# Kernel optimization log

Measured on AMD Instinct MI355X. Metric: run time of the kernel, lower is better.

Reference implementation:

```python
import jax, jax.numpy as jnp
import numpy as np

B, S, D_IN, D_OUT = 16, 2048, 512, 64
N_SLOTS = 1000  # faithful to original kernel shape; only slices 0..2 used
SCALE = 1.0 / jnp.sqrt(jnp.float32(64.0))


def setup_inputs() -> dict:
    key = jax.random.key(0)
    k1, k2 = jax.random.split(key)
    inputs = jax.random.normal(k1, (B, S, D_IN), dtype=jnp.float32)
    # keras 'uniform' initializer: U(-0.05, 0.05)
    kernel = jax.random.uniform(k2, (N_SLOTS, D_IN, D_OUT), dtype=jnp.float32,
                                minval=-0.05, maxval=0.05)
    return {"inputs": inputs, "kernel": kernel}


def reference(inputs, kernel):
    # Q, K, V projections: [B,S,D_in] @ [D_in,D_out] -> [B,S,D_out]
    q = jnp.einsum('bsi,io->bso', inputs, kernel[0])
    k = jnp.einsum('bsi,io->bso', inputs, kernel[1])
    v = jnp.einsum('bsi,io->bso', inputs, kernel[2])
    # scores: [B,S,S], scaled by 1/sqrt(64)
    scores = jnp.einsum('bqd,bkd->bqk', q, k) * SCALE
    attn = jax.nn.softmax(scores, axis=-1)
    # output: [B,S,D_out]
    return jnp.einsum('bqk,bkd->bqd', attn, v)
```

## Files before the change

### kernel.cpp

```cpp
#include <hip/hip_runtime.h>
#include <hip/hip_bf16.h>

typedef __bf16 bhalf;
typedef __attribute__((ext_vector_type(8)))  __bf16 bhalf8;
typedef __attribute__((ext_vector_type(4)))  float  f32x4;
typedef __attribute__((ext_vector_type(16))) float  f32x16;
typedef __attribute__((ext_vector_type(4)))  unsigned int u32x4;

#define NB   16
#define SEQ  2048
#define DIN  512
#define DOUT 64
#define NTOK (NB*SEQ)
#define NSPLIT 4
#define KVPER (SEQ/NSPLIT)

#define WT_BYTES (192*512*2)
#define Q_OFF    ((size_t)WT_BYTES)
#define QKV_BYTES ((size_t)NTOK*DOUT*2)
#define K_OFF    (Q_OFF + QKV_BYTES)
#define VT_OFF   (K_OFF + QKV_BYTES)

__device__ __forceinline__ void gl_lds16(const void* g, void* l) {
  __builtin_amdgcn_global_load_lds(
      (const __attribute__((address_space(1))) void*)g,
      (__attribute__((address_space(3))) void*)l, 16, 0, 0);
}

__global__ __launch_bounds__(256) void prep_w(const float* __restrict__ wk,
                                              bhalf* __restrict__ wt) {
  int tid  = blockIdx.x*256 + threadIdx.x;
  int slot = tid >> 15;
  int rem  = tid & 32767;
  int k    = rem >> 6;
  int col  = rem & 63;
  float v  = wk[tid];
  if (slot == 0) v *= 0.18033688011112042f;
  wt[(size_t)(slot*64 + col)*DIN + k] = (bhalf)v;
}

__global__ __launch_bounds__(256) void proj_qkv(const float* __restrict__ x,
    const bhalf* __restrict__ wt, bhalf* __restrict__ qb,
    bhalf* __restrict__ kb, bhalf* __restrict__ vtb) {
  __shared__ __align__(16) char smem[81920];
  char* const xs  = smem;
  char* const wsl = smem + 32768;

  const int tid  = threadIdx.x;
  const int lane = tid & 63;
  const int wv   = tid >> 6;
  const int r16  = lane & 15;
  const int g    = lane >> 4;
  const int tok0 = blockIdx.x * 64;

  const char* const xg = (const char*)(x + (size_t)tok0 * DIN);
  const char* const wg = (const char*)wt;

  auto stage = [&](int buf, int c) {
#pragma unroll
    for (int i = 0; i < 10; ++i) {
      const int p = wv*10 + i;
      if (p < 24) {
        const int n = p*8 + (lane >> 3);
        const int s = lane & 7;
        gl_lds16(wg + (size_t)n*1024 + c*128 + ((s ^ (n & 7)) << 4),
                 wsl + buf*24576 + p*1024);
      } else {
        const int q = p - 24;
        const int r = q*4 + (lane >> 4);
        const int s = lane & 15;
        gl_lds16(xg + (size_t)r*2048 + c*256 + ((s ^ (r & 7)) << 4),
                 xs + buf*16384 + q*1024);
      }
    }
  };

  f32x4 acc[12];
#pragma unroll
  for (int i = 0; i < 12; ++i) acc[i] = (f32x4){0.f, 0.f, 0.f, 0.f};

  stage(0, 0);
  __syncthreads();

  const int row = wv*16 + r16;
  const int rx7 = r16 & 7;

  int buf = 0;
  for (int c = 0; c < 8; ++c) {
    if (c < 7) stage(buf ^ 1, c + 1);
    const char* xrow = xs  + buf*16384 + row*256;
    const char* wb   = wsl + buf*24576;
#pragma unroll
    for (int kk = 0; kk < 2; ++kk) {
      const int sa = kk*8 + g*2;
      f32x4 xa = *(const f32x4*)(xrow + (( sa      ^ rx7) << 4));
      f32x4 xc = *(const f32x4*)(xrow + (((sa + 1) ^ rx7) << 4));
      bhalf8 a;
      a[0]=(bhalf)xa[0]; a[1]=(bhalf)xa[1]; a[2]=(bhalf)xa[2]; a[3]=(bhalf)xa[3];
      a[4]=(bhalf)xc[0]; a[5]=(bhalf)xc[1]; a[6]=(bhalf)xc[2]; a[7]=(bhalf)xc[3];
      const int sb = (kk*4 + g) ^ rx7;
      __builtin_amdgcn_s_setprio(1);
#pragma unroll
      for (int nt = 0; nt < 12; ++nt) {
        const bhalf8 bf = *(const bhalf8*)(wb + (nt*16 + r16)*128 + (sb << 4));
        acc[nt] = __builtin_amdgcn_mfma_f32_16x16x32_bf16(a, bf, acc[nt], 0, 0, 0);
      }
      __builtin_amdgcn_s_setprio(0);
    }
    __syncthreads();
    buf ^= 1;
  }

#pragma unroll
  for (int nt = 0; nt < 8; ++nt) {
    bhalf* dst = (nt < 4) ? qb : kb;
    const size_t base = (size_t)(nt & 3)*512 + (size_t)(r16 >> 3)*256 + (r16 & 7);
#pragma unroll
    for (int rr = 0; rr < 4; ++rr) {
      const int tok = tok0 + wv*16 + g*4 + rr;
      dst[(size_t)(tok >> 5)*2048 + base + (tok & 31)*8] = (bhalf)acc[nt][rr];
    }
  }
  auto vlds = (bhalf(*)[64][24])(void*)smem;
#pragma unroll
  for (int nt = 8; nt < 12; ++nt)
#pragma unroll
    for (int rr = 0; rr < 4; ++rr)
      vlds[wv][(nt - 8)*16 + r16][g*4 + rr] = (bhalf)acc[nt][rr];
  __syncthreads();
  {
    const int f    = lane;
    const int tokG = tok0 + wv*16;
    const int tile = tokG >> 5;
    const int s    = (tokG >> 4) & 1;
    bhalf8 v0 = *(const bhalf8*)&vlds[wv][f][0];
    bhalf8 v1 = *(const bhalf8*)&vlds[wv][f][8];
    bhalf* dstv = vtb + (size_t)tile*2048 + (size_t)(f >> 5)*1024
                      + (size_t)s*512 + (size_t)(f & 31)*8;
    *(bhalf8*)dstv         = v0;
    *(bhalf8*)(dstv + 256) = v1;
  }
}

__device__ __forceinline__ unsigned cvtpk(float lo, float hi_) {
  unsigned r;
  asm("v_cvt_pk_bf16_f32 %0, %1, %2" : "=v"(r) : "v"(lo), "v"(hi_));
  return r;
}
__device__ __forceinline__ bhalf8 mk8(unsigned a, unsigned b, unsigned c, unsigned d) {
  u32x4 u; u[0]=a; u[1]=b; u[2]=c; u[3]=d;
  return __builtin_bit_cast(bhalf8, u);
}

__global__ __launch_bounds__(256, 4) void attn(const bhalf* __restrict__ qb,
    const bhalf* __restrict__ kb, const bhalf* __restrict__ vtb,
    float* __restrict__ out) {
  __shared__ float po[NSPLIT][64][33];
  __shared__ float pl[NSPLIT][32];

  const int lane = threadIdx.x & 63;
  const int wv   = threadIdx.x >> 6;
  const int l31  = lane & 31;
  const int hi   = lane >> 5;

  const int qtile = (blockIdx.x & 7)*128 + (blockIdx.x >> 3);
  const int qbase = qtile*32;
  const int b     = qbase >> 11;
  const int kv0   = wv * KVPER;
  const int tile0 = b*64 + wv*16;

  const int fo = hi*256 + l31*8;

  const bhalf* qpk = qb + (size_t)qtile*2048 + fo;
  const bhalf8 qf0 = *(const bhalf8*)(qpk);
  const bhalf8 qf1 = *(const bhalf8*)(qpk + 512);
  const bhalf8 qf2 = *(const bhalf8*)(qpk + 1024);
  const bhalf8 qf3 = *(const bhalf8*)(qpk + 1536);

  const bhalf* kpk = kb  + (size_t)tile0*2048 + fo;
  const bhalf* vpk = vtb + (size_t)tile0*2048 + fo;

  f32x16 ot0, ot1;
#pragma unroll
  for (int r = 0; r < 16; ++r) { ot0[r] = 0.f; ot1[r] = 0.f; }
  float lsum = 0.f;

  bhalf8 kf0, kf1, kf2, kf3;
  bhalf8 vf0, vf1, vf2, vf3;
  bhalf8 pf0, pf1;
  f32x16 s;

#define LOADK(IT) do { const bhalf* p_ = kpk + (IT)*2048;                       \
    kf0 = *(const bhalf8*)(p_);          kf1 = *(const bhalf8*)(p_ + 512);      \
    kf2 = *(const bhalf8*)(p_ + 1024);   kf3 = *(const bhalf8*)(p_ + 1536); } while (0)
#define LOADV(IT) do { const bhalf* p_ = vpk + (IT)*2048;                       \
    vf0 = *(const bhalf8*)(p_);          vf1 = *(const bhalf8*)(p_ + 512);      \
    vf2 = *(const bhalf8*)(p_ + 1024);   vf3 = *(const bhalf8*)(p_ + 1536); } while (0)
#define QK() do {                                                               \
    _Pragma("unroll") for (int r_ = 0; r_ < 16; ++r_) s[r_] = 0.f;              \
    __builtin_amdgcn_s_setprio(1);                                              \
    s = __builtin_amdgcn_mfma_f32_32x32x16_bf16(kf0, qf0, s, 0, 0, 0);          \
    s = __builtin_amdgcn_mfma_f32_32x32x16_bf16(kf1, qf1, s, 0, 0, 0);          \
    s = __builtin_amdgcn_mfma_f32_32x32x16_bf16(kf2, qf2, s, 0, 0, 0);          \
    s = __builtin_amdgcn_mfma_f32_32x32x16_bf16(kf3, qf3, s, 0, 0, 0);          \
    __builtin_amdgcn_s_setprio(0); } while (0)
#define SM() do {                                                               \
    _Pragma("unroll") for (int r_ = 0; r_ < 16; ++r_)                           \
      s[r_] = __builtin_amdgcn_exp2f(s[r_]);                                    \
    lsum += ((s[0]+s[1])+(s[2]+s[3])) + ((s[4]+s[5])+(s[6]+s[7]))               \
          + ((s[8]+s[9])+(s[10]+s[11])) + ((s[12]+s[13])+(s[14]+s[15]));        \
    unsigned w0 = cvtpk(s[0],  s[1]),  w1 = cvtpk(s[2],  s[3]);                 \
    unsigned w2 = cvtpk(s[4],  s[5]),  w3 = cvtpk(s[6],  s[7]);                 \
    unsigned w4 = cvtpk(s[8],  s[9]),  w5 = cvtpk(s[10], s[11]);                \
    unsigned w6 = cvtpk(s[12], s[13]), w7 = cvtpk(s[14], s[15]);                \
    asm volatile("v_permlane32_swap_b32 %0, %1" : "+v"(w0), "+v"(w2));          \
    asm volatile("v_permlane32_swap_b32 %0, %1" : "+v"(w1), "+v"(w3));          \
    asm volatile("v_permlane32_swap_b32 %0, %1" : "+v"(w4), "+v"(w6));          \
    asm volatile("v_permlane32_swap_b32 %0, %1" : "+v"(w5), "+v"(w7));          \
    pf0 = mk8(w0, w1, w2, w3);                                                  \
    pf1 = mk8(w4, w5, w6, w7); } while (0)
#define PV() do {                                                               \
    __builtin_amdgcn_s_setprio(1);                                              \
    ot0 = __builtin_amdgcn_mfma_f32_32x32x16_bf16(vf0, pf0, ot0, 0, 0, 0);      \
    ot0 = __builtin_amdgcn_mfma_f32_32x32x16_bf16(vf1, pf1, ot0, 0, 0, 0);      \
    ot1 = __builtin_amdgcn_mfma_f32_32x32x16_bf16(vf2, pf0, ot1, 0, 0, 0);      \
    ot1 = __builtin_amdgcn_mfma_f32_32x32x16_bf16(vf3, pf1, ot1, 0, 0, 0);      \
    __builtin_amdgcn_s_setprio(0); } while (0)

  LOADK(0);
  LOADV(0);
  QK();
  LOADK(1);
  SM();

  for (int it = 0; it < KVPER/32 - 1; ++it) {
    PV();
    LOADV(it + 1);
    QK();
    if (it < KVPER/32 - 2) LOADK(it + 2);
    SM();
  }
  PV();

#undef LOADK
#undef LOADV
#undef QK
#undef SM
#undef PV

  lsum += __shfl_xor(lsum, 32);

#pragma unroll
  for (int r = 0; r < 16; ++r) {
    int d0 = (r & 3) + 8*(r >> 2) + 4*hi;
    po[wv][d0][l31]      = ot0[r];
    po[wv][32 + d0][l31] = ot1[r];
  }
  if (hi == 0) pl[wv][l31] = lsum;
  __syncthreads();

  {
    int q  = threadIdx.x >> 3;
    int dg = (threadIdx.x & 7) * 8;
    float L  = pl[0][q] + pl[1][q] + pl[2][q] + pl[3][q];
    float inv = 1.0f / L;
    float* orow = out + (size_t)(qbase + q)*DOUT + dg;
#pragma unroll
    for (int j = 0; j < 8; ++j) {
      float acc = po[0][dg+j][q] + po[1][dg+j][q]
                + po[2][dg+j][q] + po[3][dg+j][q];
      orow[j] = acc * inv;
    }
  }
}

extern "C" void kernel_launch(void* const* d_in, const int* in_sizes, int n_in,
                              void* d_out, int out_size, void* d_ws, size_t ws_size,
                              hipStream_t stream) {
  const float* x  = (const float*)d_in[0];
  const float* wk = (const float*)d_in[1];
  float* out = (float*)d_out;

  char* ws = (char*)d_ws;
  bhalf* wt = (bhalf*)(ws);
  bhalf* qq = (bhalf*)(ws + Q_OFF);
  bhalf* kk = (bhalf*)(ws + K_OFF);
  bhalf* vt = (bhalf*)(ws + VT_OFF);

  prep_w  <<<dim3(384),  dim3(256), 0, stream>>>(wk, wt);
  proj_qkv<<<dim3(512),  dim3(256), 0, stream>>>(x, wt, qq, kk, vt);
  attn    <<<dim3(1024), dim3(256), 0, stream>>>(qq, kk, vt, out);
}
```

Before: 51.07 us.

## Process two query tiles per attention block and split projection N across 8 waves

Each attention block now handles two 32-row query tiles, so every K/V fragment loaded from global memory is reused for two QK/PV chains. The grid halves to 512 blocks and the loop interleaves the two chains' MFMAs and softmax to hide latency. The projection kernel moves to 512 threads, with two wave groups splitting the 12 output column tiles, which lowers per-wave accumulator pressure and raises parallelism. The cost is more registers in attention (occupancy hint removed) and fewer attention blocks, which could under-fill the GPU.

```diff
diff --git a/kernel.cpp b/kernel.cpp
--- a/kernel.cpp
+++ b/kernel.cpp
@@ -39,7 +39,7 @@
   wt[(size_t)(slot*64 + col)*DIN + k] = (bhalf)v;
 }
 
-__global__ __launch_bounds__(256) void proj_qkv(const float* __restrict__ x,
+__global__ __launch_bounds__(512) void proj_qkv(const float* __restrict__ x,
     const bhalf* __restrict__ wt, bhalf* __restrict__ qb,
     bhalf* __restrict__ kb, bhalf* __restrict__ vtb) {
   __shared__ __align__(16) char smem[81920];
@@ -49,6 +49,8 @@
   const int tid  = threadIdx.x;
   const int lane = tid & 63;
   const int wv   = tid >> 6;
+  const int tg   = wv & 3;
+  const int ng   = wv >> 2;
   const int r16  = lane & 15;
   const int g    = lane >> 4;
   const int tok0 = blockIdx.x * 64;
@@ -58,8 +60,8 @@
 
   auto stage = [&](int buf, int c) {
 #pragma unroll
-    for (int i = 0; i < 10; ++i) {
-      const int p = wv*10 + i;
+    for (int i = 0; i < 5; ++i) {
+      const int p = wv*5 + i;
       if (p < 24) {
         const int n = p*8 + (lane >> 3);
         const int s = lane & 7;
@@ -75,14 +77,13 @@
     }
   };
 
-  f32x4 acc[12];
-#pragma unroll
-  for (int i = 0; i < 12; ++i) acc[i] = (f32x4){0.f, 0.f, 0.f, 0.f};
+  f32x4 acc0 = {0.f,0.f,0.f,0.f}, acc1 = acc0, acc2 = acc0,
+        acc3 = acc0, acc4 = acc0, acc5 = acc0;
 
   stage(0, 0);
   __syncthreads();
 
-  const int row = wv*16 + r16;
+  const int row = tg*16 + r16;
   const int rx7 = r16 & 7;
 
   int buf = 0;
@@ -100,41 +101,48 @@
       a[4]=(bhalf)xc[0]; a[5]=(bhalf)xc[1]; a[6]=(bhalf)xc[2]; a[7]=(bhalf)xc[3];
       const int sb = (kk*4 + g) ^ rx7;
       __builtin_amdgcn_s_setprio(1);
-#pragma unroll
-      for (int nt = 0; nt < 12; ++nt) {
-        const bhalf8 bf = *(const bhalf8*)(wb + (nt*16 + r16)*128 + (sb << 4));
-        acc[nt] = __builtin_amdgcn_mfma_f32_16x16x32_bf16(a, bf, acc[nt], 0, 0, 0);
-      }
+#define MF(J, ACC) do {                                                         \
+        const int nt_ = ng*6 + (J);                                             \
+        const bhalf8 bf_ = *(const bhalf8*)(wb + (nt_*16 + r16)*128 + (sb << 4)); \
+        ACC = __builtin_amdgcn_mfma_f32_16x16x32_bf16(a, bf_, ACC, 0, 0, 0);    \
+      } while (0)
+      MF(0, acc0); MF(1, acc1); MF(2, acc2);
+      MF(3, acc3); MF(4, acc4); MF(5, acc5);
+#undef MF
       __builtin_amdgcn_s_setprio(0);
     }
     __syncthreads();
     buf ^= 1;
   }
 
-#pragma unroll
-  for (int nt = 0; nt < 8; ++nt) {
-    bhalf* dst = (nt < 4) ? qb : kb;
-    const size_t base = (size_t)(nt & 3)*512 + (size_t)(r16 >> 3)*256 + (r16 & 7);
-#pragma unroll
-    for (int rr = 0; rr < 4; ++rr) {
-      const int tok = tok0 + wv*16 + g*4 + rr;
-      dst[(size_t)(tok >> 5)*2048 + base + (tok & 31)*8] = (bhalf)acc[nt][rr];
-    }
-  }
+#define STOREJ(J, ACC) do {                                                     \
+    const int nt = ng*6 + (J);                                                  \
+    if (nt < 8) {                                                               \
+      bhalf* dst = (nt < 4) ? qb : kb;                                          \
+      const size_t base = (size_t)(nt & 3)*512 + (size_t)(r16 >> 3)*256 + (r16 & 7); \
+      _Pragma("unroll")                                                         \
+      for (int rr = 0; rr < 4; ++rr) {                                          \
+        const int tok = tok0 + tg*16 + g*4 + rr;                                \
+        dst[(size_t)(tok >> 5)*2048 + base + (tok & 31)*8] = (bhalf)ACC[rr];    \
+      }                                                                         \
+    } else {                                                                    \
+      _Pragma("unroll")                                                         \
+      for (int rr = 0; rr < 4; ++rr)                                            \
+        vlds[tg][(nt - 8)*16 + r16][g*4 + rr] = (bhalf)ACC[rr];                 \
+    } } while (0)
+
   auto vlds = (bhalf(*)[64][24])(void*)smem;
-#pragma unroll
-  for (int nt = 8; nt < 12; ++nt)
-#pragma unroll
-    for (int rr = 0; rr < 4; ++rr)
-      vlds[wv][(nt - 8)*16 + r16][g*4 + rr] = (bhalf)acc[nt][rr];
-  __syncthreads();
-  {
+  STOREJ(0, acc0); STOREJ(1, acc1); STOREJ(2, acc2);
+  STOREJ(3, acc3); STOREJ(4, acc4); STOREJ(5, acc5);
+#undef STOREJ
+  __syncthreads();
+  if (ng == 1) {
     const int f    = lane;
-    const int tokG = tok0 + wv*16;
+    const int tokG = tok0 + tg*16;
     const int tile = tokG >> 5;
     const int s    = (tokG >> 4) & 1;
-    bhalf8 v0 = *(const bhalf8*)&vlds[wv][f][0];
-    bhalf8 v1 = *(const bhalf8*)&vlds[wv][f][8];
+    bhalf8 v0 = *(const bhalf8*)&vlds[tg][f][0];
+    bhalf8 v1 = *(const bhalf8*)&vlds[tg][f][8];
     bhalf* dstv = vtb + (size_t)tile*2048 + (size_t)(f >> 5)*1024
                       + (size_t)s*512 + (size_t)(f & 31)*8;
     *(bhalf8*)dstv         = v0;
@@ -152,7 +160,7 @@
   return __builtin_bit_cast(bhalf8, u);
 }
 
-__global__ __launch_bounds__(256, 4) void attn(const bhalf* __restrict__ qb,
+__global__ __launch_bounds__(256) void attn(const bhalf* __restrict__ qb,
     const bhalf* __restrict__ kb, const bhalf* __restrict__ vtb,
     float* __restrict__ out) {
   __shared__ float po[NSPLIT][64][33];
@@ -163,31 +171,35 @@
   const int l31  = lane & 31;
   const int hi   = lane >> 5;
 
-  const int qtile = (blockIdx.x & 7)*128 + (blockIdx.x >> 3);
-  const int qbase = qtile*32;
-  const int b     = qbase >> 11;
-  const int kv0   = wv * KVPER;
+  const int pr    = (blockIdx.x & 7)*64 + (blockIdx.x >> 3);
+  const int qtA   = pr*2;
+  const int qtB   = qtA + 1;
+  const int b     = qtA >> 6;
   const int tile0 = b*64 + wv*16;
-
-  const int fo = hi*256 + l31*8;
-
-  const bhalf* qpk = qb + (size_t)qtile*2048 + fo;
-  const bhalf8 qf0 = *(const bhalf8*)(qpk);
-  const bhalf8 qf1 = *(const bhalf8*)(qpk + 512);
-  const bhalf8 qf2 = *(const bhalf8*)(qpk + 1024);
-  const bhalf8 qf3 = *(const bhalf8*)(qpk + 1536);
+  const int fo    = hi*256 + l31*8;
+
+  const bhalf* qpA = qb + (size_t)qtA*2048 + fo;
+  const bhalf8 qfA0 = *(const bhalf8*)(qpA);
+  const bhalf8 qfA1 = *(const bhalf8*)(qpA + 512);
+  const bhalf8 qfA2 = *(const bhalf8*)(qpA + 1024);
+  const bhalf8 qfA3 = *(const bhalf8*)(qpA + 1536);
+  const bhalf* qpB = qb + (size_t)qtB*2048 + fo;
+  const bhalf8 qfB0 = *(const bhalf8*)(qpB);
+  const bhalf8 qfB1 = *(const bhalf8*)(qpB + 512);
+  const bhalf8 qfB2 = *(const bhalf8*)(qpB + 1024);
+  const bhalf8 qfB3 = *(const bhalf8*)(qpB + 1536);
 
   const bhalf* kpk = kb  + (size_t)tile0*2048 + fo;
   const bhalf* vpk = vtb + (size_t)tile0*2048 + fo;
 
-  f32x16 ot0, ot1;
-#pragma unroll
-  for (int r = 0; r < 16; ++r) { ot0[r] = 0.f; ot1[r] = 0.f; }
-  float lsum = 0.f;
+  f32x16 otA0, otA1, otB0, otB1;
+#pragma unroll
+  for (int r = 0; r < 16; ++r) { otA0[r]=0.f; otA1[r]=0.f; otB0[r]=0.f; otB1[r]=0.f; }
+  float lsA = 0.f, lsB = 0.f;
 
   bhalf8 kf0, kf1, kf2, kf3;
   bhalf8 vf0, vf1, vf2, vf3;
-  bhalf8 pf0, pf1;
+  bhalf8 pfA0, pfA1, pfB0, pfB1;
   f32x16 s;
 
 #define LOADK(IT) do { const bhalf* p_ = kpk + (IT)*2048;                       \
@@ -196,19 +208,19 @@
 #define LOADV(IT) do { const bhalf* p_ = vpk + (IT)*2048;                       \
     vf0 = *(const bhalf8*)(p_);          vf1 = *(const bhalf8*)(p_ + 512);      \
     vf2 = *(const bhalf8*)(p_ + 1024);   vf3 = *(const bhalf8*)(p_ + 1536); } while (0)
-#define QK() do {                                                               \
+#define QK(QF0, QF1, QF2, QF3) do {                                             \
     _Pragma("unroll") for (int r_ = 0; r_ < 16; ++r_) s[r_] = 0.f;              \
     __builtin_amdgcn_s_setprio(1);                                              \
-    s = __builtin_amdgcn_mfma_f32_32x32x16_bf16(kf0, qf0, s, 0, 0, 0);          \
-    s = __builtin_amdgcn_mfma_f32_32x32x16_bf16(kf1, qf1, s, 0, 0, 0);          \
-    s = __builtin_amdgcn_mfma_f32_32x32x16_bf16(kf2, qf2, s, 0, 0, 0);          \
-    s = __builtin_amdgcn_mfma_f32_32x32x16_bf16(kf3, qf3, s, 0, 0, 0);          \
+    s = __builtin_amdgcn_mfma_f32_32x32x16_bf16(kf0, QF0, s, 0, 0, 0);          \
+    s = __builtin_amdgcn_mfma_f32_32x32x16_bf16(kf1, QF1, s, 0, 0, 0);          \
+    s = __builtin_amdgcn_mfma_f32_32x32x16_bf16(kf2, QF2, s, 0, 0, 0);          \
+    s = __builtin_amdgcn_mfma_f32_32x32x16_bf16(kf3, QF3, s, 0, 0, 0);          \
     __builtin_amdgcn_s_setprio(0); } while (0)
-#define SM() do {                                                               \
+#define SM(PF0, PF1, LS) do {                                                   \
     _Pragma("unroll") for (int r_ = 0; r_ < 16; ++r_)                           \
       s[r_] = __builtin_amdgcn_exp2f(s[r_]);                                    \
-    lsum += ((s[0]+s[1])+(s[2]+s[3])) + ((s[4]+s[5])+(s[6]+s[7]))               \
-          + ((s[8]+s[9])+(s[10]+s[11])) + ((s[12]+s[13])+(s[14]+s[15]));        \
+    LS += ((s[0]+s[1])+(s[2]+s[3])) + ((s[4]+s[5])+(s[6]+s[7]))                 \
+        + ((s[8]+s[9])+(s[10]+s[11])) + ((s[12]+s[13])+(s[14]+s[15]));          \
     unsigned w0 = cvtpk(s[0],  s[1]),  w1 = cvtpk(s[2],  s[3]);                 \
     unsigned w2 = cvtpk(s[4],  s[5]),  w3 = cvtpk(s[6],  s[7]);                 \
     unsigned w4 = cvtpk(s[8],  s[9]),  w5 = cvtpk(s[10], s[11]);                \
@@ -217,30 +229,29 @@
     asm volatile("v_permlane32_swap_b32 %0, %1" : "+v"(w1), "+v"(w3));          \
     asm volatile("v_permlane32_swap_b32 %0, %1" : "+v"(w4), "+v"(w6));          \
     asm volatile("v_permlane32_swap_b32 %0, %1" : "+v"(w5), "+v"(w7));          \
-    pf0 = mk8(w0, w1, w2, w3);                                                  \
-    pf1 = mk8(w4, w5, w6, w7); } while (0)
-#define PV() do {                                                               \
+    PF0 = mk8(w0, w1, w2, w3);                                                  \
+    PF1 = mk8(w4, w5, w6, w7); } while (0)
+#define PV(PF0, PF1, OT0, OT1) do {                                             \
     __builtin_amdgcn_s_setprio(1);                                              \
-    ot0 = __builtin_amdgcn_mfma_f32_32x32x16_bf16(vf0, pf0, ot0, 0, 0, 0);      \
-    ot0 = __builtin_amdgcn_mfma_f32_32x32x16_bf16(vf1, pf1, ot0, 0, 0, 0);      \
-    ot1 = __builtin_amdgcn_mfma_f32_32x32x16_bf16(vf2, pf0, ot1, 0, 0, 0);      \
-    ot1 = __builtin_amdgcn_mfma_f32_32x32x16_bf16(vf3, pf1, ot1, 0, 0, 0);      \
+    OT0 = __builtin_amdgcn_mfma_f32_32x32x16_bf16(vf0, PF0, OT0, 0, 0, 0);      \
+    OT0 = __builtin_amdgcn_mfma_f32_32x32x16_bf16(vf1, PF1, OT0, 0, 0, 0);      \
+    OT1 = __builtin_amdgcn_mfma_f32_32x32x16_bf16(vf2, PF0, OT1, 0, 0, 0);      \
+    OT1 = __builtin_amdgcn_mfma_f32_32x32x16_bf16(vf3, PF1, OT1, 0, 0, 0);      \
     __builtin_amdgcn_s_setprio(0); } while (0)
 
   LOADK(0);
   LOADV(0);
-  QK();
-  LOADK(1);
-  SM();
-
-  for (int it = 0; it < KVPER/32 - 1; ++it) {
-    PV();
-    LOADV(it + 1);
-    QK();
-    if (it < KVPER/32 - 2) LOADK(it + 2);
-    SM();
-  }
-  PV();
+
+  for (int it = 0; it < KVPER/32; ++it) {
+    QK(qfA0, qfA1, qfA2, qfA3);
+    SM(pfA0, pfA1, lsA);
+    QK(qfB0, qfB1, qfB2, qfB3);
+    if (it < KVPER/32 - 1) LOADK(it + 1);
+    PV(pfA0, pfA1, otA0, otA1);
+    SM(pfB0, pfB1, lsB);
+    PV(pfB0, pfB1, otB0, otB1);
+    if (it < KVPER/32 - 1) LOADV(it + 1);
+  }
 
 #undef LOADK
 #undef LOADV
@@ -248,29 +259,47 @@
 #undef SM
 #undef PV
 
-  lsum += __shfl_xor(lsum, 32);
+  lsA += __shfl_xor(lsA, 32);
+  lsB += __shfl_xor(lsB, 32);
 
 #pragma unroll
   for (int r = 0; r < 16; ++r) {
     int d0 = (r & 3) + 8*(r >> 2) + 4*hi;
-    po[wv][d0][l31]      = ot0[r];
-    po[wv][32 + d0][l31] = ot1[r];
-  }
-  if (hi == 0) pl[wv][l31] = lsum;
-  __syncthreads();
-
+    po[wv][d0][l31]      = otA0[r];
+    po[wv][32 + d0][l31] = otA1[r];
+  }
+  if (hi == 0) pl[wv][l31] = lsA;
+  __syncthreads();
   {
     int q  = threadIdx.x >> 3;
     int dg = (threadIdx.x & 7) * 8;
-    float L  = pl[0][q] + pl[1][q] + pl[2][q] + pl[3][q];
+    float L   = pl[0][q] + pl[1][q] + pl[2][q] + pl[3][q];
     float inv = 1.0f / L;
-    float* orow = out + (size_t)(qbase + q)*DOUT + dg;
-#pragma unroll
-    for (int j = 0; j < 8; ++j) {
-      float acc = po[0][dg+j][q] + po[1][dg+j][q]
-                + po[2][dg+j][q] + po[3][dg+j][q];
-      orow[j] = acc * inv;
-    }
+    float* orow = out + (size_t)(qtA*32 + q)*DOUT + dg;
+#pragma unroll
+    for (int j = 0; j < 8; ++j)
+      orow[j] = (po[0][dg+j][q] + po[1][dg+j][q]
+               + po[2][dg+j][q] + po[3][dg+j][q]) * inv;
+  }
+  __syncthreads();
+#pragma unroll
+  for (int r = 0; r < 16; ++r) {
+    int d0 = (r & 3) + 8*(r >> 2) + 4*hi;
+    po[wv][d0][l31]      = otB0[r];
+    po[wv][32 + d0][l31] = otB1[r];
+  }
+  if (hi == 0) pl[wv][l31] = lsB;
+  __syncthreads();
+  {
+    int q  = threadIdx.x >> 3;
+    int dg = (threadIdx.x & 7) * 8;
+    float L   = pl[0][q] + pl[1][q] + pl[2][q] + pl[3][q];
+    float inv = 1.0f / L;
+    float* orow = out + (size_t)(qtB*32 + q)*DOUT + dg;
+#pragma unroll
+    for (int j = 0; j < 8; ++j)
+      orow[j] = (po[0][dg+j][q] + po[1][dg+j][q]
+               + po[2][dg+j][q] + po[3][dg+j][q]) * inv;
   }
 }
 
@@ -287,7 +316,7 @@
   bhalf* kk = (bhalf*)(ws + K_OFF);
   bhalf* vt = (bhalf*)(ws + VT_OFF);
 
-  prep_w  <<<dim3(384),  dim3(256), 0, stream>>>(wk, wt);
-  proj_qkv<<<dim3(512),  dim3(256), 0, stream>>>(x, wt, qq, kk, vt);
-  attn    <<<dim3(1024), dim3(256), 0, stream>>>(qq, kk, vt, out);
-}
+  prep_w  <<<dim3(384), dim3(256), 0, stream>>>(wk, wt);
+  proj_qkv<<<dim3(512), dim3(512), 0, stream>>>(x, wt, qq, kk, vt);
+  attn    <<<dim3(512), dim3(256), 0, stream>>>(qq, kk, vt, out);
+}
```

Result: faster. 49.55 us, median of 2 (-3.0%).

## Double block size to 512 threads in projection and attention kernels

Applied to the files above, without the earlier changes.

The projection kernel now runs 8 waves per block, splitting the 12 output column tiles into two groups of 6 across wave pairs. This halves per-wave accumulators and MFMA work and spreads staging loads over more waves. The attention kernel processes two query tiles per block, with 8 waves sharing the block and the grid halved, and writes its reduction in two phases through the shared buffer. The aim is more waves in flight to hide latency, at the cost of larger blocks, extra barriers, and a serialized epilogue that could lower occupancy or add sync overhead.

```diff
diff --git a/kernel.cpp b/kernel.cpp
--- a/kernel.cpp
+++ b/kernel.cpp
@@ -39,7 +39,7 @@
   wt[(size_t)(slot*64 + col)*DIN + k] = (bhalf)v;
 }
 
-__global__ __launch_bounds__(256) void proj_qkv(const float* __restrict__ x,
+__global__ __launch_bounds__(512) void proj_qkv(const float* __restrict__ x,
     const bhalf* __restrict__ wt, bhalf* __restrict__ qb,
     bhalf* __restrict__ kb, bhalf* __restrict__ vtb) {
   __shared__ __align__(16) char smem[81920];
@@ -49,6 +49,8 @@
   const int tid  = threadIdx.x;
   const int lane = tid & 63;
   const int wv   = tid >> 6;
+  const int tg   = wv & 3;
+  const int ng   = wv >> 2;
   const int r16  = lane & 15;
   const int g    = lane >> 4;
   const int tok0 = blockIdx.x * 64;
@@ -58,8 +60,8 @@
 
   auto stage = [&](int buf, int c) {
 #pragma unroll
-    for (int i = 0; i < 10; ++i) {
-      const int p = wv*10 + i;
+    for (int i = 0; i < 5; ++i) {
+      const int p = wv*5 + i;
       if (p < 24) {
         const int n = p*8 + (lane >> 3);
         const int s = lane & 7;
@@ -75,14 +77,13 @@
     }
   };
 
-  f32x4 acc[12];
-#pragma unroll
-  for (int i = 0; i < 12; ++i) acc[i] = (f32x4){0.f, 0.f, 0.f, 0.f};
+  f32x4 acc0 = {0.f,0.f,0.f,0.f}, acc1 = acc0, acc2 = acc0,
+        acc3 = acc0, acc4 = acc0, acc5 = acc0;
 
   stage(0, 0);
   __syncthreads();
 
-  const int row = wv*16 + r16;
+  const int row = tg*16 + r16;
   const int rx7 = r16 & 7;
 
   int buf = 0;
@@ -100,41 +101,48 @@
       a[4]=(bhalf)xc[0]; a[5]=(bhalf)xc[1]; a[6]=(bhalf)xc[2]; a[7]=(bhalf)xc[3];
       const int sb = (kk*4 + g) ^ rx7;
       __builtin_amdgcn_s_setprio(1);
-#pragma unroll
-      for (int nt = 0; nt < 12; ++nt) {
-        const bhalf8 bf = *(const bhalf8*)(wb + (nt*16 + r16)*128 + (sb << 4));
-        acc[nt] = __builtin_amdgcn_mfma_f32_16x16x32_bf16(a, bf, acc[nt], 0, 0, 0);
-      }
+#define MF(J, ACC) do {                                                         \
+        const int nt_ = ng*6 + (J);                                             \
+        const bhalf8 bf_ = *(const bhalf8*)(wb + (nt_*16 + r16)*128 + (sb << 4)); \
+        ACC = __builtin_amdgcn_mfma_f32_16x16x32_bf16(a, bf_, ACC, 0, 0, 0);    \
+      } while (0)
+      MF(0, acc0); MF(1, acc1); MF(2, acc2);
+      MF(3, acc3); MF(4, acc4); MF(5, acc5);
+#undef MF
       __builtin_amdgcn_s_setprio(0);
     }
     __syncthreads();
     buf ^= 1;
   }
 
-#pragma unroll
-  for (int nt = 0; nt < 8; ++nt) {
-    bhalf* dst = (nt < 4) ? qb : kb;
-    const size_t base = (size_t)(nt & 3)*512 + (size_t)(r16 >> 3)*256 + (r16 & 7);
-#pragma unroll
-    for (int rr = 0; rr < 4; ++rr) {
-      const int tok = tok0 + wv*16 + g*4 + rr;
-      dst[(size_t)(tok >> 5)*2048 + base + (tok & 31)*8] = (bhalf)acc[nt][rr];
-    }
-  }
+#define STOREJ(J, ACC) do {                                                     \
+    const int nt = ng*6 + (J);                                                  \
+    if (nt < 8) {                                                               \
+      bhalf* dst = (nt < 4) ? qb : kb;                                          \
+      const size_t base = (size_t)(nt & 3)*512 + (size_t)(r16 >> 3)*256 + (r16 & 7); \
+      _Pragma("unroll")                                                         \
+      for (int rr = 0; rr < 4; ++rr) {                                          \
+        const int tok = tok0 + tg*16 + g*4 + rr;                                \
+        dst[(size_t)(tok >> 5)*2048 + base + (tok & 31)*8] = (bhalf)ACC[rr];    \
+      }                                                                         \
+    } else {                                                                    \
+      _Pragma("unroll")                                                         \
+      for (int rr = 0; rr < 4; ++rr)                                            \
+        vlds[tg][(nt - 8)*16 + r16][g*4 + rr] = (bhalf)ACC[rr];                 \
+    } } while (0)
+
   auto vlds = (bhalf(*)[64][24])(void*)smem;
-#pragma unroll
-  for (int nt = 8; nt < 12; ++nt)
-#pragma unroll
-    for (int rr = 0; rr < 4; ++rr)
-      vlds[wv][(nt - 8)*16 + r16][g*4 + rr] = (bhalf)acc[nt][rr];
+  STOREJ(0, acc0); STOREJ(1, acc1); STOREJ(2, acc2);
+  STOREJ(3, acc3); STOREJ(4, acc4); STOREJ(5, acc5);
+#undef STOREJ
   __syncthreads();
-  {
+  if (ng == 1) {
     const int f    = lane;
-    const int tokG = tok0 + wv*16;
+    const int tokG = tok0 + tg*16;
     const int tile = tokG >> 5;
     const int s    = (tokG >> 4) & 1;
-    bhalf8 v0 = *(const bhalf8*)&vlds[wv][f][0];
-    bhalf8 v1 = *(const bhalf8*)&vlds[wv][f][8];
+    bhalf8 v0 = *(const bhalf8*)&vlds[tg][f][0];
+    bhalf8 v1 = *(const bhalf8*)&vlds[tg][f][8];
     bhalf* dstv = vtb + (size_t)tile*2048 + (size_t)(f >> 5)*1024
                       + (size_t)s*512 + (size_t)(f & 31)*8;
     *(bhalf8*)dstv         = v0;
@@ -152,7 +160,7 @@
   return __builtin_bit_cast(bhalf8, u);
 }
 
-__global__ __launch_bounds__(256, 4) void attn(const bhalf* __restrict__ qb,
+__global__ __launch_bounds__(512, 4) void attn(const bhalf* __restrict__ qb,
     const bhalf* __restrict__ kb, const bhalf* __restrict__ vtb,
     float* __restrict__ out) {
   __shared__ float po[NSPLIT][64][33];
@@ -160,18 +168,18 @@
 
   const int lane = threadIdx.x & 63;
   const int wv   = threadIdx.x >> 6;
+  const int sp   = wv & 3;
+  const int tl   = wv >> 2;
   const int l31  = lane & 31;
   const int hi   = lane >> 5;
 
-  const int qtile = (blockIdx.x & 7)*128 + (blockIdx.x >> 3);
-  const int qbase = qtile*32;
-  const int b     = qbase >> 11;
-  const int kv0   = wv * KVPER;
-  const int tile0 = b*64 + wv*16;
-
-  const int fo = hi*256 + l31*8;
-
-  const bhalf* qpk = qb + (size_t)qtile*2048 + fo;
+  const int pr    = (blockIdx.x & 7)*64 + (blockIdx.x >> 3);
+  const int qt    = pr*2 + tl;
+  const int b     = qt >> 6;
+  const int tile0 = b*64 + sp*16;
+  const int fo    = hi*256 + l31*8;
+
+  const bhalf* qpk = qb + (size_t)qt*2048 + fo;
   const bhalf8 qf0 = *(const bhalf8*)(qpk);
   const bhalf8 qf1 = *(const bhalf8*)(qpk + 512);
   const bhalf8 qf2 = *(const bhalf8*)(qpk + 1024);
@@ -251,26 +259,29 @@
   lsum += __shfl_xor(lsum, 32);
 
 #pragma unroll
-  for (int r = 0; r < 16; ++r) {
-    int d0 = (r & 3) + 8*(r >> 2) + 4*hi;
-    po[wv][d0][l31]      = ot0[r];
-    po[wv][32 + d0][l31] = ot1[r];
-  }
-  if (hi == 0) pl[wv][l31] = lsum;
-  __syncthreads();
-
-  {
-    int q  = threadIdx.x >> 3;
-    int dg = (threadIdx.x & 7) * 8;
-    float L  = pl[0][q] + pl[1][q] + pl[2][q] + pl[3][q];
-    float inv = 1.0f / L;
-    float* orow = out + (size_t)(qbase + q)*DOUT + dg;
-#pragma unroll
-    for (int j = 0; j < 8; ++j) {
-      float acc = po[0][dg+j][q] + po[1][dg+j][q]
-                + po[2][dg+j][q] + po[3][dg+j][q];
-      orow[j] = acc * inv;
+  for (int ph = 0; ph < 2; ++ph) {
+    if (tl == ph) {
+#pragma unroll
+      for (int r = 0; r < 16; ++r) {
+        int d0 = (r & 3) + 8*(r >> 2) + 4*hi;
+        po[sp][d0][l31]      = ot0[r];
+        po[sp][32 + d0][l31] = ot1[r];
+      }
+      if (hi == 0) pl[sp][l31] = lsum;
     }
+    __syncthreads();
+    {
+      int q  = threadIdx.x >> 4;
+      int dg = (threadIdx.x & 15) * 4;
+      float L   = pl[0][q] + pl[1][q] + pl[2][q] + pl[3][q];
+      float inv = 1.0f / L;
+      float* orow = out + (size_t)((pr*2 + ph)*32 + q)*DOUT + dg;
+#pragma unroll
+      for (int j = 0; j < 4; ++j)
+        orow[j] = (po[0][dg+j][q] + po[1][dg+j][q]
+                 + po[2][dg+j][q] + po[3][dg+j][q]) * inv;
+    }
+    if (ph == 0) __syncthreads();
   }
 }
 
@@ -287,7 +298,7 @@
   bhalf* kk = (bhalf*)(ws + K_OFF);
   bhalf* vt = (bhalf*)(ws + VT_OFF);
 
-  prep_w  <<<dim3(384),  dim3(256), 0, stream>>>(wk, wt);
-  proj_qkv<<<dim3(512),  dim3(256), 0, stream>>>(x, wt, qq, kk, vt);
-  attn    <<<dim3(1024), dim3(256), 0, stream>>>(qq, kk, vt, out);
-}
+  prep_w  <<<dim3(384), dim3(256), 0, stream>>>(wk, wt);
+  proj_qkv<<<dim3(512), dim3(512), 0, stream>>>(x, wt, qq, kk, vt);
+  attn    <<<dim3(512), dim3(512), 0, stream>>>(qq, kk, vt, out);
+}
```

New measurement: 51.85 us. No clear change (+1.5%).
